# Performance work log

Measured on AMD Instinct MI355X. Metric: run time of the kernel, lower is better.

Reference implementation:

```python
import jax, jax.numpy as jnp
import numpy as np

EPS = 1e-5

def _bn(x, g, b):
    # BatchNorm1d over nodes (training-mode batch statistics), per channel
    m = x.mean(0)
    v = x.var(0)
    return (x - m) / jnp.sqrt(v + EPS) * g + b

def _ln(x, g, b):
    # per-node LayerNorm over feature dim
    m = x.mean(-1, keepdims=True)
    v = x.var(-1, keepdims=True)
    return (x - m) / jnp.sqrt(v + EPS) * g + b

def _gcn(x, src, dst, n, W, b):
    # GCNConv: x @ W, symmetric deg^-1/2 normalization (self loops already in src/dst), scatter-add at dst
    xw = x @ W  # [N, C]
    deg = jax.ops.segment_sum(jnp.ones_like(src, dtype=x.dtype), dst, num_segments=n)
    dinv = jnp.where(deg > 0, 1.0 / jnp.sqrt(deg), 0.0)
    coef = (dinv[src] * dinv[dst])[:, None]  # [E+N, 1]
    return jax.ops.segment_sum(xw[src] * coef, dst, num_segments=n) + b

def _attn(x, Wqkv, bqkv, Wo, bo):
    # nn.MultiheadAttention, heads=1, single graph (batch=None) -> dense N x N attention
    C = x.shape[-1]
    qkv = x @ Wqkv.T + bqkv  # [N, 3C]
    q, k, v = jnp.split(qkv, 3, axis=-1)
    s = (q @ k.T) / jnp.sqrt(jnp.asarray(C, x.dtype))  # [N, N]
    a = jax.nn.softmax(s, axis=-1)
    return (a @ v) @ Wo.T + bo

def setup_inputs() -> dict:
    N, E, IN, C, L, OUT = 8192, 131072, 128, 64, 4, 21
    key = jax.random.key(0)
    ks = jax.random.split(key, 12)
    s = lambda i, shape, sc=0.05: jax.random.normal(ks[i], shape, jnp.float32) * sc
    f32 = jnp.float32
    return {
        "x": jax.random.normal(ks[0], (N, IN), f32),
        "edge_index": jax.random.randint(ks[1], (2, E), 0, N),
        "W_in": s(2, (IN, C)), "b_in": jnp.zeros((C,), f32),
        "gcn_W": s(3, (L, C, C)), "gcn_b": jnp.zeros((L, C), f32),
        "attn_Wqkv": s(4, (L, 3 * C, C)), "attn_bqkv": jnp.zeros((L, 3 * C), f32),
        "attn_Wo": s(5, (L, C, C)), "attn_bo": jnp.zeros((L, C), f32),
        "bn1_g": jnp.ones((L, C), f32), "bn1_b": jnp.zeros((L, C), f32),
        "bn2_g": jnp.ones((L, C), f32), "bn2_b": jnp.zeros((L, C), f32),
        "bn3_g": jnp.ones((L, C), f32), "bn3_b": jnp.zeros((L, C), f32),
        "mlp_W1": s(6, (L, C, 2 * C)), "mlp_b1": jnp.zeros((L, 2 * C), f32),
        "mlp_W2": s(7, (L, 2 * C, C)), "mlp_b2": jnp.zeros((L, C), f32),
        "ln_g": jnp.ones((L, C), f32), "ln_b": jnp.zeros((L, C), f32),
        "W_out": s(8, (C, OUT)), "b_out": jnp.zeros((OUT,), f32),
    }

def reference(x, edge_index, W_in, b_in, gcn_W, gcn_b, attn_Wqkv, attn_bqkv,
              attn_Wo, attn_bo, bn1_g, bn1_b, bn2_g, bn2_b, bn3_g, bn3_b,
              mlp_W1, mlp_b1, mlp_W2, mlp_b2, ln_g, ln_b, W_out, b_out):
    N = x.shape[0]
    L = gcn_W.shape[0]
    loop = jnp.arange(N, dtype=edge_index.dtype)  # self loops (GCNConv default)
    src = jnp.concatenate([edge_index[0], loop])
    dst = jnp.concatenate([edge_index[1], loop])

    h = x @ W_in + b_in  # input_transform
    for l in range(L):
        # GPSConv: local GCN branch + residual + BN (dropout=0.0 default inside GPSConv)
        h1 = _bn(_gcn(h, src, dst, N, gcn_W[l], gcn_b[l]) + h, bn1_g[l], bn1_b[l])
        # global attention branch + residual + BN
        h2 = _bn(_attn(h, attn_Wqkv[l], attn_bqkv[l], attn_Wo[l], attn_bo[l]) + h,
                 bn2_g[l], bn2_b[l])
        out = h1 + h2
        mlp = jax.nn.relu(out @ mlp_W1[l] + mlp_b1[l]) @ mlp_W2[l] + mlp_b2[l]
        out = _bn(out + mlp, bn3_g[l], bn3_b[l])
        # outer loop: LayerNorm -> relu (dropout = identity in eval)
        h = jax.nn.relu(_ln(out, ln_g[l], ln_b[l]))
    return jax.nn.log_softmax(h @ W_out + b_out, axis=1)
```

## Files before the change

### kernel.cpp

```cpp
#include <hip/hip_runtime.h>
#include <math.h>

#define NN 8192
#define NE 131072
#define CIN 128
#define C 64
#define NL 4
#define COUT 21
#define EPSV 1e-5f
#define ALPHA 0.18033688011112043f

typedef unsigned short u16;
typedef __attribute__((ext_vector_type(8))) short short8;
typedef __attribute__((ext_vector_type(4))) float f32x4;
typedef __attribute__((ext_vector_type(4))) unsigned int u32x4;
typedef __attribute__((ext_vector_type(2))) unsigned int u32x2;

__device__ __forceinline__ u16 f2bf(float x) {
  unsigned int u = __float_as_uint(x);
  u += 0x7FFF + ((u >> 16) & 1);
  return (u16)(u >> 16);
}

__device__ __forceinline__ unsigned cvtpk(float a, float b) {
  unsigned r;
  asm("v_cvt_pk_bf16_f32 %0, %1, %2" : "=v"(r) : "v"(a), "v"(b));
  return r;
}

__device__ __forceinline__ int pcmap(int c) {
  return (c & 32) | (c & 3) | (((c >> 2) & 3) << 3) | (((c >> 4) & 1) << 2);
}

__device__ __forceinline__ int pc128(int c) {
  return (c & 96) | (c & 3) | (((c >> 2) & 3) << 3) | (((c >> 4) & 1) << 2);
}

__global__ void zero_setup(float* __restrict__ stats, int* __restrict__ degi) {
  int i = blockIdx.x * 256 + threadIdx.x;
  if (i < 1536) stats[i] = 0.f;
  if (i < NN) degi[i] = 0;
}

__global__ void deg_kernel(const int* __restrict__ dst, int* __restrict__ degi) {
  int e = blockIdx.x * 256 + threadIdx.x;
  if (e < NE) atomicAdd(&degi[dst[e]], 1);
}

__global__ __launch_bounds__(256) void prefix_kernel(const int* __restrict__ degi,
                                                     int* __restrict__ rowptr,
                                                     int* __restrict__ cursor) {
  __shared__ int part[256];
  int t = threadIdx.x;
  int base = t * 32;
  int loc[32];
  int s = 0;
#pragma unroll
  for (int i = 0; i < 32; ++i) { loc[i] = s; s += degi[base + i]; }
  part[t] = s;
  __syncthreads();
  for (int off = 1; off < 256; off <<= 1) {
    int v = (t >= off) ? part[t - off] : 0;
    __syncthreads();
    part[t] += v;
    __syncthreads();
  }
  int chunkbase = (t == 0) ? 0 : part[t - 1];
#pragma unroll
  for (int i = 0; i < 32; ++i) {
    int v = chunkbase + loc[i];
    rowptr[base + i] = v;
    cursor[base + i] = v;
  }
  if (t == 255) rowptr[NN] = part[255];
}

__global__ void dinv_kernel(const int* __restrict__ degi, float* __restrict__ dinv) {
  int i = blockIdx.x * 256 + threadIdx.x;
  if (i < NN) dinv[i] = rsqrtf((float)degi[i] + 1.0f);
}

__global__ void fill_kernel(const int* __restrict__ src, const int* __restrict__ dst,
                            const float* __restrict__ dinv,
                            int* __restrict__ cursor, int* __restrict__ esrc,
                            float* __restrict__ ewt) {
  int e = blockIdx.x * 256 + threadIdx.x;
  if (e < NE) {
    int d = dst[e];
    int s = src[e];
    int pos = atomicAdd(&cursor[d], 1);
    esrc[pos] = s;
    ewt[pos] = dinv[s];
  }
}

__global__ void prep_weights(const float* __restrict__ Wqkv, const float* __restrict__ Wo,
                             const float* __restrict__ Wg,
                             const float* __restrict__ W1, const float* __restrict__ W2,
                             u16* __restrict__ Wqp, u16* __restrict__ Wop,
                             u16* __restrict__ Wgp,
                             u16* __restrict__ W1p, u16* __restrict__ W2p) {
  int idx = blockIdx.x * 256 + threadIdx.x;
  if (idx < NL * 192 * 64) {
    int l = idx / 12288, rem = idx % 12288;
    int j = rem >> 6, c = rem & 63;
    Wqp[l * 12288 + j * 64 + pcmap(c)] = f2bf(Wqkv[idx]);
  } else if (idx < NL * 192 * 64 + NL * 64 * 64) {
    int i2 = idx - NL * 192 * 64;
    int l = i2 >> 12, m = (i2 >> 6) & 63, k = i2 & 63;
    Wop[l * 4096 + m * 64 + pcmap(k)] = f2bf(Wo[i2]);
  } else if (idx < NL * 192 * 64 + 2 * NL * 64 * 64) {
    int i3 = idx - NL * 192 * 64 - NL * 64 * 64;
    int l = i3 >> 12, k = (i3 >> 6) & 63, c = i3 & 63;
    Wgp[l * 4096 + c * 64 + pcmap(k)] = f2bf(Wg[i3]);
  } else if (idx < NL * 192 * 64 + 2 * NL * 64 * 64 + NL * 64 * 128) {
    int i4 = idx - (NL * 192 * 64 + 2 * NL * 64 * 64);
    int l = i4 >> 13, i3 = i4 & 8191;
    int k = i3 >> 7, m = i3 & 127;
    W1p[l * 8192 + m * 64 + pcmap(k)] = f2bf(W1[i4]);
  } else if (idx < NL * 192 * 64 + 2 * NL * 64 * 64 + 2 * NL * 64 * 128) {
    int i5 = idx - (NL * 192 * 64 + 2 * NL * 64 * 64 + NL * 64 * 128);
    int l = i5 >> 13, i3 = i5 & 8191;
    int k = i3 >> 6, m = i3 & 63;
    W2p[l * 8192 + m * 128 + pc128(k)] = f2bf(W2[i5]);
  }
}

__global__ __launch_bounds__(256) void gemm_in_kernel(const float* __restrict__ X,
                                                      const float* __restrict__ W,
                                                      const float* __restrict__ b,
                                                      float* __restrict__ Y,
                                                      u16* __restrict__ hb) {
  int idx = blockIdx.x * 256 + threadIdx.x;
  int n = idx >> 6, c = idx & 63;
  const float* xr = X + n * CIN;
  float acc = b[c];
#pragma unroll 16
  for (int k = 0; k < CIN; ++k) acc = fmaf(xr[k], W[k * C + c], acc);
  Y[idx] = acc;
  hb[n * 64 + pcmap(c)] = f2bf(acc);
}

__global__ __launch_bounds__(128) void proj_mfma(const u16* __restrict__ hb,
                                                 const float* __restrict__ h,
                                                 const u16* __restrict__ Wqp,
                                                 const u16* __restrict__ Wgp,
                                                 const float* __restrict__ bq,
                                                 const float* __restrict__ gb,
                                                 const float* __restrict__ dinv,
                                                 u16* __restrict__ Qb,
                                                 u16* __restrict__ Kb,
                                                 u16* __restrict__ Vt,
                                                 float* __restrict__ xw,
                                                 float* __restrict__ t1) {
  __shared__ u16 ldsv[64 * 17];
  const int tid = threadIdx.x;
  const int lane = tid & 63, w = tid >> 6;
  const int r = lane & 15, q = lane >> 4;
  const int n0 = blockIdx.x * 16;
  const int n = n0 + r;

  short8 hf[2];
#pragma unroll
  for (int s = 0; s < 2; ++s)
    hf[s] = *(const short8*)(hb + (size_t)n * 64 + s * 32 + q * 8);

  if (w == 0) {
    float di = dinv[n];
#pragma unroll
    for (int jt = 0; jt < 4; ++jt) {
      f32x4 a = {};
#pragma unroll
      for (int s = 0; s < 2; ++s) {
        short8 wf = *(const short8*)(Wgp + (jt * 16 + r) * 64 + s * 32 + q * 8);
        a = __builtin_amdgcn_mfma_f32_16x16x32_bf16(wf, hf[s], a, 0, 0, 0);
      }
      int j0 = jt * 16 + q * 4;
      f32x4 hres = *(const f32x4*)&h[(size_t)n * 64 + j0];
      f32x4 gbv = *(const f32x4*)&gb[j0];
      *(f32x4*)&xw[(size_t)n * 64 + j0] = a;
      *(f32x4*)&t1[(size_t)n * 64 + j0] = a * di * di + gbv + hres;
    }
#pragma unroll
    for (int jt = 0; jt < 4; ++jt) {
      f32x4 a = {};
#pragma unroll
      for (int s = 0; s < 2; ++s) {
        short8 wf = *(const short8*)(Wqp + (jt * 16 + r) * 64 + s * 32 + q * 8);
        a = __builtin_amdgcn_mfma_f32_16x16x32_bf16(wf, hf[s], a, 0, 0, 0);
      }
      f32x4 v = (a + *(const f32x4*)&bq[jt * 16 + q * 4]) * ALPHA;
      int pb = ((jt & 2) << 4) | (q << 3) | ((jt & 1) << 2);
      *(u32x2*)(Qb + (size_t)n * 64 + pb) = u32x2{cvtpk(v[0], v[1]), cvtpk(v[2], v[3])};
    }
  } else {
#pragma unroll
    for (int jt = 0; jt < 4; ++jt) {
      f32x4 a = {};
#pragma unroll
      for (int s = 0; s < 2; ++s) {
        short8 wf = *(const short8*)(Wqp + (64 + jt * 16 + r) * 64 + s * 32 + q * 8);
        a = __builtin_amdgcn_mfma_f32_16x16x32_bf16(wf, hf[s], a, 0, 0, 0);
      }
      f32x4 v = a + *(const f32x4*)&bq[64 + jt * 16 + q * 4];
      int pb = ((jt & 2) << 4) | (q << 3) | ((jt & 1) << 2);
      *(u32x2*)(Kb + (size_t)n * 64 + pb) = u32x2{cvtpk(v[0], v[1]), cvtpk(v[2], v[3])};
    }
#pragma unroll
    for (int jt = 0; jt < 4; ++jt) {
      f32x4 a = {};
#pragma unroll
      for (int s = 0; s < 2; ++s) {
        short8 wf = *(const short8*)(Wqp + (128 + jt * 16 + r) * 64 + s * 32 + q * 8);
        a = __builtin_amdgcn_mfma_f32_16x16x32_bf16(wf, hf[s], a, 0, 0, 0);
      }
      f32x4 v = a + *(const f32x4*)&bq[128 + jt * 16 + q * 4];
      int j0 = jt * 16 + q * 4;
#pragma unroll
      for (int e = 0; e < 4; ++e) ldsv[(j0 + e) * 17 + r] = f2bf(v[e]);
    }
  }
  __syncthreads();

  const int d = tid >> 1, cp = tid & 1;
  const int grp = n0 & ~31, hh = (n0 >> 4) & 1;
#pragma unroll
  for (int ci = 0; ci < 2; ++ci) {
    int cc = cp * 2 + ci;
    u16 a0 = ldsv[d * 17 + cc * 4 + 0];
    u16 a1 = ldsv[d * 17 + cc * 4 + 1];
    u16 a2 = ldsv[d * 17 + cc * 4 + 2];
    u16 a3 = ldsv[d * 17 + cc * 4 + 3];
    *(u32x2*)(Vt + (size_t)d * NN + grp + cc * 8 + hh * 4) =
        u32x2{(unsigned)a0 | ((unsigned)a1 << 16), (unsigned)a2 | ((unsigned)a3 << 16)};
  }
}

__global__ __launch_bounds__(256) void gcn_gather(const int* __restrict__ rowptr,
                                                  const int* __restrict__ esrc,
                                                  const float* __restrict__ ewt,
                                                  const float* __restrict__ xw,
                                                  const float* __restrict__ dinv,
                                                  float* __restrict__ t1,
                                                  float* __restrict__ stats) {
  __shared__ float gs[4][64], gss[4][64];
  int w = threadIdx.x >> 6, lane = threadIdx.x & 63;
  float s = 0.f, ss = 0.f;
#pragma unroll
  for (int rr = 0; rr < 2; ++rr) {
    int d = blockIdx.x * 8 + w * 2 + rr;
    int beg = rowptr[d], end = rowptr[d + 1];
    float acc = 0.f;
    int i = beg;
    for (; i + 4 <= end; i += 4) {
      int s0 = esrc[i], s1 = esrc[i + 1], s2 = esrc[i + 2], s3 = esrc[i + 3];
      float w0 = ewt[i], w1 = ewt[i + 1], w2 = ewt[i + 2], w3 = ewt[i + 3];
      float x0 = xw[(size_t)s0 * 64 + lane];
      float x1 = xw[(size_t)s1 * 64 + lane];
      float x2 = xw[(size_t)s2 * 64 + lane];
      float x3 = xw[(size_t)s3 * 64 + lane];
      acc = fmaf(x0, w0, acc);
      acc = fmaf(x1, w1, acc);
      acc = fmaf(x2, w2, acc);
      acc = fmaf(x3, w3, acc);
    }
    for (; i < end; ++i) acc = fmaf(xw[(size_t)esrc[i] * 64 + lane], ewt[i], acc);
    size_t idx = (size_t)d * 64 + lane;
    float v = t1[idx] + acc * dinv[d];
    t1[idx] = v;
    s += v; ss += v * v;
  }
  gs[w][lane] = s; gss[w][lane] = ss;
  __syncthreads();
  int t = threadIdx.x;
  if (t < 64) atomicAdd(&stats[t], gs[0][t] + gs[1][t] + gs[2][t] + gs[3][t]);
  else if (t < 128) {
    int c = t - 64;
    atomicAdd(&stats[64 + c], gss[0][c] + gss[1][c] + gss[2][c] + gss[3][c]);
  }
}

__device__ __forceinline__ void loadK(short8 (&kf)[8], const u16* kb, int koff) {
#pragma unroll
  for (int jt = 0; jt < 4; ++jt)
#pragma unroll
    for (int s = 0; s < 2; ++s)
      kf[jt * 2 + s] = *(const short8*)(kb + koff + jt * 1024 + s * 32);
}

__device__ __forceinline__ void loadV(short8 (&vf)[8], const u16* vb, int voff) {
#pragma unroll
  for (int dt = 0; dt < 4; ++dt)
#pragma unroll
    for (int s = 0; s < 2; ++s)
      vf[dt * 2 + s] = *(const short8*)(vb + voff + dt * 16 * NN + s * 32);
}

__device__ __forceinline__ void computeTile(const short8 (&kf)[8], const short8 (&vf)[8],
                                            const short8 (&qf)[4][2],
                                            f32x4 (&o)[4][4], float (&ll)[4]) {
#pragma unroll
  for (int pair = 0; pair < 2; ++pair) {
    f32x4 st[2][4] = {};
#pragma unroll
    for (int s = 0; s < 2; ++s)
#pragma unroll
      for (int jp = 0; jp < 2; ++jp) {
        short8 kfrag = kf[(pair * 2 + jp) * 2 + s];
#pragma unroll
        for (int it = 0; it < 4; ++it)
          st[jp][it] = __builtin_amdgcn_mfma_f32_16x16x32_bf16(kfrag, qf[it][s], st[jp][it], 0, 0, 0);
      }
    short8 pf[4];
#pragma unroll
    for (int it = 0; it < 4; ++it) {
      float p[8];
#pragma unroll
      for (int jp = 0; jp < 2; ++jp)
#pragma unroll
        for (int r = 0; r < 4; ++r) p[jp * 4 + r] = exp2f(st[jp][it][r]);
      ll[it] += ((p[0] + p[1]) + (p[2] + p[3])) + ((p[4] + p[5]) + (p[6] + p[7]));
      u32x4 a;
      a[0] = cvtpk(p[0], p[1]); a[1] = cvtpk(p[2], p[3]);
      a[2] = cvtpk(p[4], p[5]); a[3] = cvtpk(p[6], p[7]);
      pf[it] = __builtin_bit_cast(short8, a);
    }
#pragma unroll
    for (int dt = 0; dt < 4; ++dt) {
      short8 vfrag = vf[dt * 2 + pair];
#pragma unroll
      for (int it = 0; it < 4; ++it)
        o[dt][it] = __builtin_amdgcn_mfma_f32_16x16x32_bf16(vfrag, pf[it], o[dt][it], 0, 0, 0);
    }
  }
}

__global__ __launch_bounds__(512, 2)
void attn_mfma(const u16* __restrict__ Qb, const u16* __restrict__ Kb,
               const u16* __restrict__ Vtb, float* __restrict__ Opart,
               float* __restrict__ Lpart) {
  __shared__ float fsm[2 * 64 * 68 + 2 * 64];
  const int tid = threadIdx.x;
  const int lane = tid & 63;
  const int w = tid >> 6;
  const int qt = blockIdx.x >> 1, ks = blockIdx.x & 1;
  const int qbase = qt * 64;
  const int kv0 = ks * 4096 + w * 512;
  const int r = lane & 15, q = lane >> 4;

  short8 qf[4][2];
#pragma unroll
  for (int it = 0; it < 4; ++it)
#pragma unroll
    for (int s = 0; s < 2; ++s)
      qf[it][s] = *(const short8*)(Qb + (size_t)(qbase + it * 16 + r) * 64 + s * 32 + q * 8);

  f32x4 o[4][4] = {};
  float ll[4] = {0.f, 0.f, 0.f, 0.f};

  const u16* kb = Kb + (size_t)(kv0 + r) * 64 + q * 8;
  const u16* vb = Vtb + (size_t)r * NN + kv0 + q * 8;

  short8 kA[8], kB[8], vf[8];
  loadK(kA, kb, 0);
#pragma unroll 1
  for (int t = 0; t < 8; t += 2) {
    loadV(vf, vb, t * 64);
    loadK(kB, kb, (t + 1) * 4096);
    computeTile(kA, vf, qf, o, ll);
    loadV(vf, vb, (t + 1) * 64);
    if (t + 2 < 8) loadK(kA, kb, (t + 2) * 4096);
    computeTile(kB, vf, qf, o, ll);
  }

#pragma unroll
  for (int it = 0; it < 4; ++it) {
    ll[it] += __shfl_xor(ll[it], 16);
    ll[it] += __shfl_xor(ll[it], 32);
  }

  float* buf = fsm + (w & 1) * (64 * 68);
  float* lb = fsm + 2 * 64 * 68 + (w & 1) * 64;
  for (int rr = 0; rr < 4; ++rr) {
    if ((w >> 1) == rr) {
      if (rr == 0) {
#pragma unroll
        for (int dt = 0; dt < 4; ++dt)
#pragma unroll
          for (int it = 0; it < 4; ++it)
            *(f32x4*)&buf[(it * 16 + r) * 68 + dt * 16 + q * 4] = o[dt][it];
        if (lane < 16)
#pragma unroll
          for (int it = 0; it < 4; ++it) lb[it * 16 + lane] = ll[it];
      } else {
#pragma unroll
        for (int dt = 0; dt < 4; ++dt)
#pragma unroll
          for (int it = 0; it < 4; ++it) {
            float* p = &buf[(it * 16 + r) * 68 + dt * 16 + q * 4];
            *(f32x4*)p = *(const f32x4*)p + o[dt][it];
          }
        if (lane < 16)
#pragma unroll
          for (int it = 0; it < 4; ++it) lb[it * 16 + lane] += ll[it];
      }
    }
    __syncthreads();
  }

  int row = tid >> 3, d0 = (tid & 7) * 8;
  float* outp = Opart + (size_t)(qt * 2 + ks) * 4096 + row * 64 + d0;
  const float* b0 = fsm + row * 68 + d0;
  const float* b1 = b0 + 64 * 68;
#pragma unroll
  for (int j = 0; j < 8; ++j) outp[j] = b0[j] + b1[j];
  if (tid < 64)
    Lpart[(qt * 2 + ks) * 64 + tid] = fsm[2 * 64 * 68 + tid] + fsm[2 * 64 * 68 + 64 + tid];
}

__global__ __launch_bounds__(256) void oproj_mfma(const float* __restrict__ Opart,
                                                  const float* __restrict__ Lpart,
                                                  const u16* __restrict__ Wop,
                                                  const float* __restrict__ bo,
                                                  const float* __restrict__ res,
                                                  float* __restrict__ Y,
                                                  float* __restrict__ stats) {
  __shared__ u16 ldso[32 * 72];
  __shared__ float os[2][64], oss[2][64];
  const int tid = threadIdx.x;
  const int n0 = blockIdx.x * 32;
  const int qtile = n0 >> 6;

  {
    int row = tid >> 3, c0 = (tid & 7) * 8;
    int r64 = (n0 + row) & 63;
    float inv = 1.f / (Lpart[qtile * 128 + r64] + Lpart[qtile * 128 + 64 + r64]);
    const float* O0 = Opart + (size_t)(qtile * 2) * 4096 + r64 * 64;
    const float* O1 = O0 + 4096;
#pragma unroll
    for (int j8 = 0; j8 < 2; ++j8) {
      f32x4 a = *(const f32x4*)&O0[c0 + j8 * 4];
      f32x4 b = *(const f32x4*)&O1[c0 + j8 * 4];
      f32x4 vsum = (a + b) * inv;
#pragma unroll
      for (int e = 0; e < 4; ++e) ldso[row * 72 + pcmap(c0 + j8 * 4 + e)] = f2bf(vsum[e]);
    }
  }
  __syncthreads();

  const int lane = tid & 63, w = tid >> 6;
  const int r = lane & 15, q = lane >> 4;
  const int ntile = w & 1, mhalf = w >> 1;
  short8 hf[2];
#pragma unroll
  for (int s = 0; s < 2; ++s)
    hf[s] = *(const short8*)&ldso[(ntile * 16 + r) * 72 + s * 32 + q * 8];

  const int n = n0 + ntile * 16 + r;
#pragma unroll
  for (int mi = 0; mi < 2; ++mi) {
    int mt = mhalf * 2 + mi;
    f32x4 a = {};
#pragma unroll
    for (int s = 0; s < 2; ++s) {
      short8 wf = *(const short8*)(Wop + (mt * 16 + r) * 64 + s * 32 + q * 8);
      a = __builtin_amdgcn_mfma_f32_16x16x32_bf16(wf, hf[s], a, 0, 0, 0);
    }
    int m0 = mt * 16 + q * 4;
    f32x4 out = a + *(const f32x4*)&bo[m0] + *(const f32x4*)&res[(size_t)n * 64 + m0];
    *(f32x4*)&Y[(size_t)n * 64 + m0] = out;
    f32x4 s_ = out, q_ = out * out;
#pragma unroll
    for (int off = 1; off < 16; off <<= 1) {
#pragma unroll
      for (int e = 0; e < 4; ++e) {
        s_[e] += __shfl_xor(s_[e], off);
        q_[e] += __shfl_xor(q_[e], off);
      }
    }
    if (r == 0) {
#pragma unroll
      for (int e = 0; e < 4; ++e) {
        os[ntile][m0 + e] = s_[e];
        oss[ntile][m0 + e] = q_[e];
      }
    }
  }
  __syncthreads();
  if (tid < 64) atomicAdd(&stats[tid], os[0][tid] + os[1][tid]);
  else if (tid < 128) {
    int c = tid - 64;
    atomicAdd(&stats[64 + c], oss[0][c] + oss[1][c]);
  }
}

__global__ __launch_bounds__(256) void mlp_mfma(const float* __restrict__ t1,
                                                const float* __restrict__ t0,
                                                const float* __restrict__ s1,
                                                const float* __restrict__ s2,
                                                const float* __restrict__ g1,
                                                const float* __restrict__ bb1,
                                                const float* __restrict__ g2,
                                                const float* __restrict__ bb2,
                                                const u16* __restrict__ W1p,
                                                const float* __restrict__ b1,
                                                const u16* __restrict__ W2p,
                                                const float* __restrict__ b2,
                                                float* __restrict__ t4,
                                                float* __restrict__ stats) {
  __shared__ float rows[32][68];
  __shared__ u16 xb[32 * 72];
  __shared__ u16 midb[32 * 136];
  __shared__ float os[2][64], oss[2][64];
  int t = threadIdx.x;
  int r0 = blockIdx.x * 32;

  for (int i = t; i < 2048; i += 256) {
    int rr = i >> 6, c = i & 63;
    int idx = (r0 + rr) * 64 + c;
    float m1 = s1[c] * (1.f / NN);
    float v1 = s1[64 + c] * (1.f / NN) - m1 * m1;
    float m2 = s2[c] * (1.f / NN);
    float v2 = s2[64 + c] * (1.f / NN) - m2 * m2;
    float val = (t1[idx] - m1) * rsqrtf(v1 + EPSV) * g1[c] + bb1[c] +
                (t0[idx] - m2) * rsqrtf(v2 + EPSV) * g2[c] + bb2[c];
    rows[rr][c] = val;
    xb[rr * 72 + pcmap(c)] = f2bf(val);
  }
  __syncthreads();

  const int lane = t & 63, w = t >> 6;
  const int r = lane & 15, q = lane >> 4;
  const int ntile = w & 1, mgrp = w >> 1;

  short8 hf[2];
#pragma unroll
  for (int s = 0; s < 2; ++s)
    hf[s] = *(const short8*)&xb[(ntile * 16 + r) * 72 + s * 32 + q * 8];

#pragma unroll
  for (int mi = 0; mi < 4; ++mi) {
    int mt = mgrp * 4 + mi;
    f32x4 a = {};
#pragma unroll
    for (int s = 0; s < 2; ++s) {
      short8 wf = *(const short8*)(W1p + (mt * 16 + r) * 64 + s * 32 + q * 8);
      a = __builtin_amdgcn_mfma_f32_16x16x32_bf16(wf, hf[s], a, 0, 0, 0);
    }
    int m0 = mt * 16 + q * 4;
    f32x4 v = a + *(const f32x4*)&b1[m0];
#pragma unroll
    for (int e = 0; e < 4; ++e)
      midb[(ntile * 16 + r) * 136 + pc128(m0 + e)] = f2bf(fmaxf(v[e], 0.f));
  }
  __syncthreads();

  short8 mf[4];
#pragma unroll
  for (int s = 0; s < 4; ++s)
    mf[s] = *(const short8*)&midb[(ntile * 16 + r) * 136 + s * 32 + q * 8];

  const int n = r0 + ntile * 16 + r;
#pragma unroll
  for (int mi = 0; mi < 2; ++mi) {
    int mt = mgrp * 2 + mi;
    f32x4 a = {};
#pragma unroll
    for (int s = 0; s < 4; ++s) {
      short8 wf = *(const short8*)(W2p + (mt * 16 + r) * 128 + s * 32 + q * 8);
      a = __builtin_amdgcn_mfma_f32_16x16x32_bf16(wf, mf[s], a, 0, 0, 0);
    }
    int m0 = mt * 16 + q * 4;
    f32x4 out = a + *(const f32x4*)&b2[m0] + *(const f32x4*)&rows[ntile * 16 + r][m0];
    *(f32x4*)&t4[(size_t)n * 64 + m0] = out;
    f32x4 s_ = out, q_ = out * out;
#pragma unroll
    for (int off = 1; off < 16; off <<= 1) {
#pragma unroll
      for (int e = 0; e < 4; ++e) {
        s_[e] += __shfl_xor(s_[e], off);
        q_[e] += __shfl_xor(q_[e], off);
      }
    }
    if (r == 0) {
#pragma unroll
      for (int e = 0; e < 4; ++e) {
        os[ntile][m0 + e] = s_[e];
        oss[ntile][m0 + e] = q_[e];
      }
    }
  }
  __syncthreads();
  if (t < 64) atomicAdd(&stats[t], os[0][t] + os[1][t]);
  else if (t < 128) {
    int c = t - 64;
    atomicAdd(&stats[64 + c], oss[0][c] + oss[1][c]);
  }
}

__global__ __launch_bounds__(256) void bn3_ln_relu(const float* __restrict__ t4,
                                                   const float* __restrict__ s3,
                                                   const float* __restrict__ g3,
                                                   const float* __restrict__ b3,
                                                   const float* __restrict__ lg,
                                                   const float* __restrict__ lb,
                                                   float* __restrict__ H,
                                                   u16* __restrict__ hb) {
  int wv = threadIdx.x >> 6, lane = threadIdx.x & 63;
  int n = blockIdx.x * 4 + wv;
  float m3 = s3[lane] * (1.f / NN);
  float v3 = s3[64 + lane] * (1.f / NN) - m3 * m3;
  float x = (t4[n * 64 + lane] - m3) * rsqrtf(v3 + EPSV) * g3[lane] + b3[lane];
  float s = x, ss = x * x;
  for (int o = 32; o > 0; o >>= 1) {
    s += __shfl_xor(s, o, 64);
    ss += __shfl_xor(ss, o, 64);
  }
  float m = s * (1.f / 64), v = ss * (1.f / 64) - m * m;
  float y = (x - m) * rsqrtf(v + EPSV) * lg[lane] + lb[lane];
  y = fmaxf(y, 0.f);
  H[n * 64 + lane] = y;
  hb[n * 64 + pcmap(lane)] = f2bf(y);
}

__global__ __launch_bounds__(256) void final_kernel(const float* __restrict__ H,
                                                    const float* __restrict__ Wout,
                                                    const float* __restrict__ bout,
                                                    float* __restrict__ out) {
  int w = threadIdx.x >> 6, lane = threadIdx.x & 63;
  int n = blockIdx.x * 4 + w;
  const float* hr = H + n * 64;
  float acc = (lane < COUT) ? bout[lane] : -INFINITY;
  if (lane < COUT) {
#pragma unroll 16
    for (int k = 0; k < 64; ++k) acc = fmaf(hr[k], Wout[k * COUT + lane], acc);
  }
  float mx = acc;
  for (int o = 32; o > 0; o >>= 1) mx = fmaxf(mx, __shfl_xor(mx, o, 64));
  float e = __expf(acc - mx);
  float se = e;
  for (int o = 32; o > 0; o >>= 1) se += __shfl_xor(se, o, 64);
  float lse = mx + logf(se);
  if (lane < COUT) out[n * COUT + lane] = acc - lse;
}

extern "C" void kernel_launch(void* const* d_in, const int* in_sizes, int n_in,
                              void* d_out, int out_size, void* d_ws, size_t ws_size,
                              hipStream_t stream) {
  const float* x    = (const float*)d_in[0];
  const int*   ei   = (const int*)d_in[1];
  const float* W_in = (const float*)d_in[2];
  const float* b_in = (const float*)d_in[3];
  const float* gcnW = (const float*)d_in[4];
  const float* gcnB = (const float*)d_in[5];
  const float* Wqkv = (const float*)d_in[6];
  const float* bqkv = (const float*)d_in[7];
  const float* Wo   = (const float*)d_in[8];
  const float* bo   = (const float*)d_in[9];
  const float* bn1g = (const float*)d_in[10];
  const float* bn1b = (const float*)d_in[11];
  const float* bn2g = (const float*)d_in[12];
  const float* bn2b = (const float*)d_in[13];
  const float* bn3g = (const float*)d_in[14];
  const float* bn3b = (const float*)d_in[15];
  const float* W1   = (const float*)d_in[16];
  const float* b1   = (const float*)d_in[17];
  const float* W2   = (const float*)d_in[18];
  const float* b2   = (const float*)d_in[19];
  const float* lng  = (const float*)d_in[20];
  const float* lnb  = (const float*)d_in[21];
  const float* Wout = (const float*)d_in[22];
  const float* bout = (const float*)d_in[23];

  const int* src = ei;
  const int* dst = ei + NE;

  const int NC = NN * C;
  float* ws = (float*)d_ws;
  float* h     = ws + 0 * NC;
  float* t0    = ws + 1 * NC;
  float* t1    = ws + 2 * NC;
  float* Opart = ws + 3 * NC;
  float* t4    = ws + 5 * NC;
  u16* Qb  = (u16*)(ws + 6 * NC);
  u16* Kb  = Qb + NC;
  u16* Vtb = Kb + NC;
  u16* hbb = Vtb + NC;
  u16* Wqp = hbb + NC;
  u16* Wop = Wqp + NL * 192 * 64;
  u16* Wgp = Wop + NL * 64 * 64;
  u16* W1p = Wgp + NL * 64 * 64;
  u16* W2p = W1p + NL * 128 * 64;
  float* dinv = (float*)(W2p + NL * 64 * 128);
  float* statsAll = dinv + NN;
  float* Lpart = statsAll + 1536;
  int* degi   = (int*)(Lpart + 16384);
  int* rowptr = degi + NN;
  int* cursor = rowptr + NN + 8;
  int* esrc   = cursor + NN;
  float* ewt  = (float*)(esrc + NE);

  dim3 B(256);

  zero_setup<<<32, B, 0, stream>>>(statsAll, degi);
  deg_kernel<<<NE / 256, B, 0, stream>>>(dst, degi);
  prefix_kernel<<<1, B, 0, stream>>>(degi, rowptr, cursor);
  dinv_kernel<<<NN / 256, B, 0, stream>>>(degi, dinv);
  fill_kernel<<<NE / 256, B, 0, stream>>>(src, dst, dinv, cursor, esrc, ewt);
  prep_weights<<<576, B, 0, stream>>>(Wqkv, Wo, gcnW, W1, W2, Wqp, Wop, Wgp, W1p, W2p);

  gemm_in_kernel<<<NN * C / 256, B, 0, stream>>>(x, W_in, b_in, h, hbb);

  for (int l = 0; l < NL; ++l) {
    float* s1 = statsAll + l * 384;
    float* s2 = s1 + 128;
    float* s3 = s1 + 256;

    proj_mfma<<<NN / 16, 128, 0, stream>>>(hbb, h, Wqp + l * 192 * 64, Wgp + l * 4096,
                                           bqkv + l * 192, gcnB + l * C, dinv,
                                           Qb, Kb, Vtb, t0, t1);
    gcn_gather<<<NN / 8, B, 0, stream>>>(rowptr, esrc, ewt, t0, dinv, t1, s1);

    attn_mfma<<<256, 512, 0, stream>>>(Qb, Kb, Vtb, Opart, Lpart);
    oproj_mfma<<<NN / 32, B, 0, stream>>>(Opart, Lpart, Wop + l * 4096, bo + l * C, h, t0, s2);

    mlp_mfma<<<NN / 32, B, 0, stream>>>(t1, t0, s1, s2, bn1g + l * C, bn1b + l * C,
                                        bn2g + l * C, bn2b + l * C,
                                        W1p + l * 8192, b1 + l * 2 * C,
                                        W2p + l * 8192, b2 + l * C, t4, s3);
    bn3_ln_relu<<<NN / 4, B, 0, stream>>>(t4, s3, bn3g + l * C, bn3b + l * C,
                                          lng + l * C, lnb + l * C, h, hbb);
  }

  final_kernel<<<NN / 4, B, 0, stream>>>(h, Wout, bout, (float*)d_out);
}
```

Before: 529.4 us.

## Fuse GCN gather into attention kernel launch to overlap with MFMA work

Merges the GCN neighbor-gather kernel into the attention kernel as extra blocks (index 256 and up), so the memory-bound gather runs alongside the compute-bound attention blocks in one launch. This removes one launch per layer and lets the gather fill idle compute units during attention. In exchange, gather blocks now use 512-thread blocks with the attention kernel's launch bounds and register allocation. Block scheduling order may also delay the attention blocks.

```diff
diff --git a/kernel.cpp b/kernel.cpp
--- a/kernel.cpp
+++ b/kernel.cpp
@@ -236,50 +236,6 @@
   }
 }
 
-__global__ __launch_bounds__(256) void gcn_gather(const int* __restrict__ rowptr,
-                                                  const int* __restrict__ esrc,
-                                                  const float* __restrict__ ewt,
-                                                  const float* __restrict__ xw,
-                                                  const float* __restrict__ dinv,
-                                                  float* __restrict__ t1,
-                                                  float* __restrict__ stats) {
-  __shared__ float gs[4][64], gss[4][64];
-  int w = threadIdx.x >> 6, lane = threadIdx.x & 63;
-  float s = 0.f, ss = 0.f;
-#pragma unroll
-  for (int rr = 0; rr < 2; ++rr) {
-    int d = blockIdx.x * 8 + w * 2 + rr;
-    int beg = rowptr[d], end = rowptr[d + 1];
-    float acc = 0.f;
-    int i = beg;
-    for (; i + 4 <= end; i += 4) {
-      int s0 = esrc[i], s1 = esrc[i + 1], s2 = esrc[i + 2], s3 = esrc[i + 3];
-      float w0 = ewt[i], w1 = ewt[i + 1], w2 = ewt[i + 2], w3 = ewt[i + 3];
-      float x0 = xw[(size_t)s0 * 64 + lane];
-      float x1 = xw[(size_t)s1 * 64 + lane];
-      float x2 = xw[(size_t)s2 * 64 + lane];
-      float x3 = xw[(size_t)s3 * 64 + lane];
-      acc = fmaf(x0, w0, acc);
-      acc = fmaf(x1, w1, acc);
-      acc = fmaf(x2, w2, acc);
-      acc = fmaf(x3, w3, acc);
-    }
-    for (; i < end; ++i) acc = fmaf(xw[(size_t)esrc[i] * 64 + lane], ewt[i], acc);
-    size_t idx = (size_t)d * 64 + lane;
-    float v = t1[idx] + acc * dinv[d];
-    t1[idx] = v;
-    s += v; ss += v * v;
-  }
-  gs[w][lane] = s; gss[w][lane] = ss;
-  __syncthreads();
-  int t = threadIdx.x;
-  if (t < 64) atomicAdd(&stats[t], gs[0][t] + gs[1][t] + gs[2][t] + gs[3][t]);
-  else if (t < 128) {
-    int c = t - 64;
-    atomicAdd(&stats[64 + c], gss[0][c] + gss[1][c] + gss[2][c] + gss[3][c]);
-  }
-}
-
 __device__ __forceinline__ void loadK(short8 (&kf)[8], const u16* kb, int koff) {
 #pragma unroll
   for (int jt = 0; jt < 4; ++jt)
@@ -336,13 +292,64 @@
 }
 
 __global__ __launch_bounds__(512, 2)
-void attn_mfma(const u16* __restrict__ Qb, const u16* __restrict__ Kb,
-               const u16* __restrict__ Vtb, float* __restrict__ Opart,
-               float* __restrict__ Lpart) {
+void attn_gather(const u16* __restrict__ Qb, const u16* __restrict__ Kb,
+                 const u16* __restrict__ Vtb, float* __restrict__ Opart,
+                 float* __restrict__ Lpart,
+                 const int* __restrict__ rowptr, const int* __restrict__ esrc,
+                 const float* __restrict__ ewt, const float* __restrict__ xw,
+                 const float* __restrict__ dinv, float* __restrict__ t1,
+                 float* __restrict__ stats) {
   __shared__ float fsm[2 * 64 * 68 + 2 * 64];
   const int tid = threadIdx.x;
   const int lane = tid & 63;
   const int w = tid >> 6;
+
+  if (blockIdx.x >= 256) {
+    const int bid2 = blockIdx.x - 256;
+    float* gs = fsm;
+    float* gss = fsm + 512;
+    float s = 0.f, ss = 0.f;
+#pragma unroll
+    for (int rr = 0; rr < 2; ++rr) {
+      int d = bid2 * 16 + w * 2 + rr;
+      int beg = rowptr[d], end = rowptr[d + 1];
+      float acc = 0.f;
+      int i = beg;
+      for (; i + 4 <= end; i += 4) {
+        int s0 = esrc[i], s1 = esrc[i + 1], s2 = esrc[i + 2], s3 = esrc[i + 3];
+        float w0 = ewt[i], w1 = ewt[i + 1], w2 = ewt[i + 2], w3 = ewt[i + 3];
+        float x0 = xw[(size_t)s0 * 64 + lane];
+        float x1 = xw[(size_t)s1 * 64 + lane];
+        float x2 = xw[(size_t)s2 * 64 + lane];
+        float x3 = xw[(size_t)s3 * 64 + lane];
+        acc = fmaf(x0, w0, acc);
+        acc = fmaf(x1, w1, acc);
+        acc = fmaf(x2, w2, acc);
+        acc = fmaf(x3, w3, acc);
+      }
+      for (; i < end; ++i) acc = fmaf(xw[(size_t)esrc[i] * 64 + lane], ewt[i], acc);
+      size_t idx = (size_t)d * 64 + lane;
+      float v = t1[idx] + acc * dinv[d];
+      t1[idx] = v;
+      s += v; ss += v * v;
+    }
+    gs[w * 64 + lane] = s; gss[w * 64 + lane] = ss;
+    __syncthreads();
+    if (tid < 64) {
+      float a = 0.f;
+#pragma unroll
+      for (int j = 0; j < 8; ++j) a += gs[j * 64 + tid];
+      atomicAdd(&stats[tid], a);
+    } else if (tid < 128) {
+      int c = tid - 64;
+      float a = 0.f;
+#pragma unroll
+      for (int j = 0; j < 8; ++j) a += gss[j * 64 + c];
+      atomicAdd(&stats[64 + c], a);
+    }
+    return;
+  }
+
   const int qt = blockIdx.x >> 1, ks = blockIdx.x & 1;
   const int qbase = qt * 64;
   const int kv0 = ks * 4096 + w * 512;
@@ -719,9 +726,9 @@
     proj_mfma<<<NN / 16, 128, 0, stream>>>(hbb, h, Wqp + l * 192 * 64, Wgp + l * 4096,
                                            bqkv + l * 192, gcnB + l * C, dinv,
                                            Qb, Kb, Vtb, t0, t1);
-    gcn_gather<<<NN / 8, B, 0, stream>>>(rowptr, esrc, ewt, t0, dinv, t1, s1);
-
-    attn_mfma<<<256, 512, 0, stream>>>(Qb, Kb, Vtb, Opart, Lpart);
+
+    attn_gather<<<768, 512, 0, stream>>>(Qb, Kb, Vtb, Opart, Lpart,
+                                         rowptr, esrc, ewt, t0, dinv, t1, s1);
     oproj_mfma<<<NN / 32, B, 0, stream>>>(Opart, Lpart, Wop + l * 4096, bo + l * C, h, t0, s2);
 
     mlp_mfma<<<NN / 32, B, 0, stream>>>(t1, t0, s1, s2, bn1g + l * C, bn1b + l * C,
```

After: 470.4 us. 1.13x faster.
